# Performance work log

Measured on AMD Instinct MI355X. Metric: run time of the kernel, lower is better.

The kernel has to match this reference:

```python
import jax, jax.numpy as jnp
import numpy as np

N_NODES = 102
EDGES = [[0,6],[0,5],[6,8],[5,7],[0,31],[31,32],[32,33],[28,33],[28,29],[29,30],[30,31],[0,43],[40,41],[41,42],[42,43],[43,44],[44,45],[45,46],[46,47],[47,48],[48,49],[49,50],[50,51],[40,51],[40,52],[46,56],[52,53],[53,54],[54,55],[55,56],[56,57],[57,58],[58,59],[52,59],[0,34],[34,35],[35,36],[36,37],[37,38],[38,39],[34,39],[7,60],[60,61],[61,62],[62,63],[63,64],[60,65],[65,66],[66,67],[67,68],[60,69],[69,70],[70,71],[71,72],[60,73],[73,74],[74,75],[75,76],[60,77],[77,78],[78,79],[79,80],[8,81],[81,82],[82,83],[83,84],[84,85],[81,86],[86,87],[87,88],[88,89],[81,90],[90,91],[91,92],[92,93],[81,94],[94,95],[95,96],[96,97],[81,98],[98,99],[99,100],[100,101]]


def _gcn_norm_adj(edge_index):
    # PyG GCNConv: add self-loops, symmetric normalization.
    # deg computed over target (col) index including self-loops.
    row, col = edge_index[0], edge_index[1]
    deg = jnp.zeros((N_NODES,), jnp.float32).at[col].add(1.0) + 1.0  # +1 for self-loop
    dinv = jnp.where(deg > 0, 1.0 / jnp.sqrt(deg), 0.0)
    norm = dinv[row] * dinv[col]
    # out[col] += norm * x[row]  ->  A[col, row] = norm; self-loops on diagonal.
    A = jnp.zeros((N_NODES, N_NODES), jnp.float32).at[col, row].add(norm)
    A = A + jnp.diag(dinv * dinv)
    return A


def setup_inputs() -> dict:
    key = jax.random.key(0)
    k1, k2, k3, k4, k5 = jax.random.split(key, 5)
    B, n = 32, 256
    hidden, embed = 256, 256
    x = jax.random.normal(k1, (B, n, N_NODES * 2), jnp.float32)
    W_gnn = jax.random.normal(k2, (2, hidden), jnp.float32) * 0.5
    b_gnn = jax.random.normal(k3, (hidden,), jnp.float32) * 0.1
    W_proj = jax.random.normal(k4, (hidden, embed), jnp.float32) * (1.0 / np.sqrt(hidden))
    b_proj = jax.random.normal(k5, (embed,), jnp.float32) * 0.1
    edge_index = jnp.asarray(np.array(EDGES, dtype=np.int32).T)  # [2, 84]
    return {"x": x, "W_gnn": W_gnn, "b_gnn": b_gnn,
            "W_proj": W_proj, "b_proj": b_proj, "edge_index": edge_index}


def reference(x, W_gnn, b_gnn, W_proj, b_proj, edge_index):
    B, n, _ = x.shape
    xf = x.reshape(B, n, N_NODES, 2)                      # [B, n, 102, 2]
    A = _gcn_norm_adj(edge_index)                         # [102, 102]
    xw = jnp.einsum('bnuc,ch->bnuh', xf, W_gnn)           # transform
    h = jnp.einsum('vu,bnuh->bnvh', A, xw) + b_gnn        # propagate + bias
    h = jax.nn.relu(h)
    out = jnp.einsum('bnvh,he->bnve', h, W_proj) + b_proj # [B, n, 102, embed]
    return out
```

## Files before the change

### kernel.cpp

```cpp
#include <hip/hip_runtime.h>

#define N_NODES 102
#define NP 8192
#define RBLOCKS 3264
#define RSTRIDE 128

typedef _Float16 f16x8 __attribute__((ext_vector_type(8)));
typedef _Float16 f16x2 __attribute__((ext_vector_type(2)));
typedef float f32x4 __attribute__((ext_vector_type(4)));

__global__ void build_tables(const int* __restrict__ ei, int ne,
                             int4* __restrict__ gtu, float4* __restrict__ gtw) {
    __shared__ int   deg[N_NODES];
    __shared__ float dinv[N_NODES];
    __shared__ int   cnt[N_NODES];
    __shared__ int   tu[N_NODES][4];
    __shared__ float tw[N_NODES][4];
    int t = threadIdx.x;
    if (t < N_NODES) deg[t] = 1;
    __syncthreads();
    if (t == 0) for (int e = 0; e < ne; ++e) deg[ei[ne + e]] += 1;
    __syncthreads();
    if (t < N_NODES) {
        dinv[t] = 1.0f / sqrtf((float)deg[t]);
        cnt[t] = 1;
        for (int j = 0; j < 4; ++j) { tu[t][j] = 2 * t; tw[t][j] = 0.0f; }
    }
    __syncthreads();
    if (t < N_NODES) tw[t][0] = dinv[t] * dinv[t];
    __syncthreads();
    if (t == 0) {
        for (int e = 0; e < ne; ++e) {
            int r = ei[e], c = ei[ne + e];
            int s = cnt[c] < 4 ? cnt[c] : 3;
            cnt[c] = s + 1;
            tu[c][s] = 2 * r;
            tw[c][s] = dinv[r] * dinv[c];
        }
    }
    __syncthreads();
    if (t < N_NODES) {
        gtu[t] = make_int4(tu[t][0], tu[t][1], tu[t][2], tu[t][3]);
        gtw[t] = make_float4(tw[t][0], tw[t][1], tw[t][2], tw[t][3]);
    }
}

__global__ void prep_w(const float* __restrict__ Wp, _Float16* __restrict__ WpT) {
    int tid = blockIdx.x * 256 + threadIdx.x;
    for (int i = tid; i < 65536; i += 16384) {
        int col = i & 255, k = i >> 8;
        WpT[col * 256 + k] = (_Float16)Wp[i];
    }
}

__global__ __launch_bounds__(256, 2) void gnn_main(
    const float* __restrict__ x,
    const _Float16* __restrict__ WpT,
    const int4*  __restrict__ gtu,
    const float4* __restrict__ gtw,
    const float* __restrict__ Wg,
    const float* __restrict__ bg,
    const float* __restrict__ bp,
    float* __restrict__ out)
{
    __shared__ float xs[4 * 2 * N_NODES];
    __shared__ int4   stu[N_NODES];
    __shared__ float4 stw[N_NODES];
    __shared__ _Float16 W0l[256], W1l[256], bgl[256];
    const int tid = threadIdx.x;
    const int w  = tid >> 6;
    const int l  = tid & 63;
    const int qk = l >> 4;
    const int m  = l & 15;
    const int c0  = blockIdx.y * 64;
    const int rbi = blockIdx.x;

    f16x8 bfragR[8][4];
    #pragma unroll
    for (int t = 0; t < 8; ++t)
        #pragma unroll
        for (int nt = 0; nt < 4; ++nt)
            bfragR[t][nt] = *reinterpret_cast<const f16x8*>(
                &WpT[(c0 + nt * 16 + m) * 256 + qk * 8 + 32 * t]);

    if (tid < N_NODES) { stu[tid] = gtu[tid]; stw[tid] = gtw[tid]; }
    W0l[tid] = (_Float16)Wg[tid];
    W1l[tid] = (_Float16)Wg[256 + tid];
    bgl[tid] = (_Float16)bg[tid];

    float bpf[4];
    #pragma unroll
    for (int nt = 0; nt < 4; ++nt) bpf[nt] = bp[c0 + nt * 16 + m];

    const f16x2 z2 = (f16x2){ (_Float16)0.0f, (_Float16)0.0f };

    #pragma unroll 1
    for (int j = 0; j < 26; ++j) {
        const int rb = rbi + j * RSTRIDE;
        if (rb >= RBLOCKS) break;
        const int rowblk = rb * 256;
        const int pbase  = rowblk / N_NODES;

        __syncthreads();
        #pragma unroll
        for (int pi = 0; pi < 4; ++pi) {
            int p = pbase + pi;
            if (tid < 2 * N_NODES)
                xs[pi * 2 * N_NODES + tid] = (p < NP) ? x[(size_t)p * (2 * N_NODES) + tid] : 0.0f;
        }
        __syncthreads();

        f16x2 y0pk[4], y1pk[4];
        #pragma unroll
        for (int s = 0; s < 4; ++s) {
            int r = rowblk + w * 64 + s * 16 + m;
            int p = r / N_NODES;
            int v = r - p * N_NODES;
            const float* xp = &xs[(p - pbase) * 2 * N_NODES];
            int4  U = stu[v];
            float4 W = stw[v];
            float a0 = W.x * xp[U.x]     + W.y * xp[U.y]
                     + W.z * xp[U.z]     + W.w * xp[U.w];
            float a1 = W.x * xp[U.x + 1] + W.y * xp[U.y + 1]
                     + W.z * xp[U.z + 1] + W.w * xp[U.w + 1];
            _Float16 h0 = (_Float16)a0;
            _Float16 h1 = (_Float16)a1;
            y0pk[s] = (f16x2){ h0, h0 };
            y1pk[s] = (f16x2){ h1, h1 };
        }

        f32x4 acc[4][4];
        #pragma unroll
        for (int s = 0; s < 4; ++s)
            #pragma unroll
            for (int nt = 0; nt < 4; ++nt)
                acc[s][nt] = (f32x4){0.f, 0.f, 0.f, 0.f};

        #pragma unroll
        for (int t = 0; t < 8; ++t) {
            const int kk = qk * 8 + 32 * t;
            union { f16x8 v; f16x2 p[4]; } w0u, w1u, bbu;
            w0u.v = *reinterpret_cast<const f16x8*>(&W0l[kk]);
            w1u.v = *reinterpret_cast<const f16x8*>(&W1l[kk]);
            bbu.v = *reinterpret_cast<const f16x8*>(&bgl[kk]);
            #pragma unroll
            for (int s = 0; s < 4; ++s) {
                union { f16x8 v; f16x2 p[4]; } af;
                #pragma unroll
                for (int j2 = 0; j2 < 4; ++j2) {
                    f16x2 h = w0u.p[j2] * y0pk[s] + w1u.p[j2] * y1pk[s] + bbu.p[j2];
                    af.p[j2] = __builtin_elementwise_max(h, z2);
                }
                #pragma unroll
                for (int nt = 0; nt < 4; ++nt)
                    acc[s][nt] = __builtin_amdgcn_mfma_f32_16x16x32_f16(af.v, bfragR[t][nt], acc[s][nt], 0, 0, 0);
            }
        }

        const long rowbase = (long)rowblk + (long)w * 64;
        #pragma unroll
        for (int s = 0; s < 4; ++s) {
            #pragma unroll
            for (int nt = 0; nt < 4; ++nt) {
                const int e = c0 + nt * 16 + m;
                #pragma unroll
                for (int reg = 0; reg < 4; ++reg) {
                    long r = rowbase + s * 16 + qk * 4 + reg;
                    out[r * 256 + e] = acc[s][nt][reg] + bpf[nt];
                }
            }
        }
    }
}

extern "C" void kernel_launch(void* const* d_in, const int* in_sizes, int n_in,
                              void* d_out, int out_size, void* d_ws, size_t ws_size,
                              hipStream_t stream) {
    const float* x  = (const float*)d_in[0];
    const float* Wg = (const float*)d_in[1];
    const float* bg = (const float*)d_in[2];
    const float* Wp = (const float*)d_in[3];
    const float* bp = (const float*)d_in[4];
    const int* ei   = (const int*)d_in[5];
    float* out = (float*)d_out;

    const int ne = in_sizes[5] / 2;

    int4*     gtu = (int4*)d_ws;
    float4*   gtw = (float4*)((char*)d_ws + 2048);
    _Float16* WpT = (_Float16*)((char*)d_ws + 4096);

    build_tables<<<1, 128, 0, stream>>>(ei, ne, gtu, gtw);
    prep_w<<<64, 256, 0, stream>>>(Wp, WpT);

    gnn_main<<<dim3(RSTRIDE, 4), 256, 0, stream>>>(x, WpT, gtu, gtw, Wg, bg, bp, out);
}
```

Measured before the change: 199.5 us.

## Warp-specialize: dedicate one wavefront to double-buffered x prefetch

Splits the block so three wavefronts do compute and MFMA on 192-row blocks while the fourth wavefront prefetches the next x window into a double-buffered LDS area. The per-iteration pair of syncthreads is replaced by a single barrier, so global loads of x overlap with compute. In exchange, a quarter of the wavefronts no longer do compute, giving fewer MFMA rows per block, and there are more iterations per block (34 instead of up to 26).

Result: slower. 284.9 us (+42.8%).

```diff
diff --git a/kernel.cpp b/kernel.cpp
--- a/kernel.cpp
+++ b/kernel.cpp
@@ -2,8 +2,10 @@
 
 #define N_NODES 102
 #define NP 8192
-#define RBLOCKS 3264
-#define RSTRIDE 128
+#define RB192 4352
+#define GRIDX 128
+#define NITER 34
+#define XWIN 612
 
 typedef _Float16 f16x8 __attribute__((ext_vector_type(8)));
 typedef _Float16 f16x2 __attribute__((ext_vector_type(2)));
@@ -63,7 +65,7 @@
     const float* __restrict__ bp,
     float* __restrict__ out)
 {
-    __shared__ float xs[4 * 2 * N_NODES];
+    __shared__ float xsb[2][XWIN];
     __shared__ int4   stu[N_NODES];
     __shared__ float4 stw[N_NODES];
     __shared__ _Float16 W0l[256], W1l[256], bgl[256];
@@ -74,14 +76,17 @@
     const int m  = l & 15;
     const int c0  = blockIdx.y * 64;
     const int rbi = blockIdx.x;
+    const size_t gmax = (size_t)NP * (2 * N_NODES);
 
     f16x8 bfragR[8][4];
-    #pragma unroll
-    for (int t = 0; t < 8; ++t)
+    if (w < 3) {
         #pragma unroll
-        for (int nt = 0; nt < 4; ++nt)
-            bfragR[t][nt] = *reinterpret_cast<const f16x8*>(
-                &WpT[(c0 + nt * 16 + m) * 256 + qk * 8 + 32 * t]);
+        for (int t = 0; t < 8; ++t)
+            #pragma unroll
+            for (int nt = 0; nt < 4; ++nt)
+                bfragR[t][nt] = *reinterpret_cast<const f16x8*>(
+                    &WpT[(c0 + nt * 16 + m) * 256 + qk * 8 + 32 * t]);
+    }
 
     if (tid < N_NODES) { stu[tid] = gtu[tid]; stw[tid] = gtw[tid]; }
     W0l[tid] = (_Float16)Wg[tid];
@@ -92,84 +97,113 @@
     #pragma unroll
     for (int nt = 0; nt < 4; ++nt) bpf[nt] = bp[c0 + nt * 16 + m];
 
+    if (w == 3) {
+        const int pb0 = (rbi * 192) / N_NODES;
+        const size_t gbase = (size_t)pb0 * (2 * N_NODES);
+        #pragma unroll
+        for (int i = 0; i < 10; ++i) {
+            int idx = l + i * 64;
+            if (idx < XWIN)
+                xsb[0][idx] = (gbase + idx < gmax) ? x[gbase + idx] : 0.0f;
+        }
+    }
+    __syncthreads();
+
     const f16x2 z2 = (f16x2){ (_Float16)0.0f, (_Float16)0.0f };
 
     #pragma unroll 1
-    for (int j = 0; j < 26; ++j) {
-        const int rb = rbi + j * RSTRIDE;
-        if (rb >= RBLOCKS) break;
-        const int rowblk = rb * 256;
-        const int pbase  = rowblk / N_NODES;
-
-        __syncthreads();
-        #pragma unroll
-        for (int pi = 0; pi < 4; ++pi) {
-            int p = pbase + pi;
-            if (tid < 2 * N_NODES)
-                xs[pi * 2 * N_NODES + tid] = (p < NP) ? x[(size_t)p * (2 * N_NODES) + tid] : 0.0f;
+    for (int j = 0; j < NITER; ++j) {
+        const int rb = rbi + j * GRIDX;
+        const int cur = j & 1;
+
+        if (w < 3) {
+            const int rowblk = rb * 192;
+            const int pbase  = rowblk / N_NODES;
+            const float* xsw = xsb[cur];
+
+            f16x2 y0pk[4], y1pk[4];
+            #pragma unroll
+            for (int s = 0; s < 4; ++s) {
+                int r = rowblk + w * 64 + s * 16 + m;
+                int p = r / N_NODES;
+                int v = r - p * N_NODES;
+                const float* xp = &xsw[(p - pbase) * 2 * N_NODES];
+                int4  U = stu[v];
+                float4 W = stw[v];
+                float a0 = W.x * xp[U.x]     + W.y * xp[U.y]
+                         + W.z * xp[U.z]     + W.w * xp[U.w];
+                float a1 = W.x * xp[U.x + 1] + W.y * xp[U.y + 1]
+                         + W.z * xp[U.z + 1] + W.w * xp[U.w + 1];
+                _Float16 h0 = (_Float16)a0;
+                _Float16 h1 = (_Float16)a1;
+                y0pk[s] = (f16x2){ h0, h0 };
+                y1pk[s] = (f16x2){ h1, h1 };
+            }
+
+            f32x4 acc[4][4];
+            #pragma unroll
+            for (int s = 0; s < 4; ++s)
+                #pragma unroll
+                for (int nt = 0; nt < 4; ++nt)
+                    acc[s][nt] = (f32x4){0.f, 0.f, 0.f, 0.f};
+
+            #pragma unroll
+            for (int t = 0; t < 8; ++t) {
+                const int kk = qk * 8 + 32 * t;
+                union { f16x8 v; f16x2 p[4]; } w0u, w1u, bbu;
+                w0u.v = *reinterpret_cast<const f16x8*>(&W0l[kk]);
+                w1u.v = *reinterpret_cast<const f16x8*>(&W1l[kk]);
+                bbu.v = *reinterpret_cast<const f16x8*>(&bgl[kk]);
+                #pragma unroll
+                for (int s = 0; s < 4; ++s) {
+                    union { f16x8 v; f16x2 p[4]; } af;
+                    #pragma unroll
+                    for (int j2 = 0; j2 < 4; ++j2) {
+                        f16x2 h = w0u.p[j2] * y0pk[s] + w1u.p[j2] * y1pk[s] + bbu.p[j2];
+                        af.p[j2] = __builtin_elementwise_max(h, z2);
+                    }
+                    #pragma unroll
+                    for (int nt = 0; nt < 4; ++nt)
+                        acc[s][nt] = __builtin_amdgcn_mfma_f32_16x16x32_f16(af.v, bfragR[t][nt], acc[s][nt], 0, 0, 0);
+                }
+            }
+
+            const long rowbase = (long)rowblk + (long)w * 64;
+            #pragma unroll
+            for (int s = 0; s < 4; ++s) {
+                #pragma unroll
+                for (int nt = 0; nt < 4; ++nt) {
+                    const int e = c0 + nt * 16 + m;
+                    #pragma unroll
+                    for (int reg = 0; reg < 4; ++reg) {
+                        long r = rowbase + s * 16 + qk * 4 + reg;
+                        out[r * 256 + e] = acc[s][nt][reg] + bpf[nt];
+                    }
+                }
+            }
+        } else {
+            if (j + 1 < NITER) {
+                const int rbn = rbi + (j + 1) * GRIDX;
+                const int pbn = (rbn * 192) / N_NODES;
+                const size_t gbase = (size_t)pbn * (2 * N_NODES);
+                float tmp[10];
+                #pragma unroll
+                for (int i = 0; i < 10; ++i) {
+                    int idx = l + i * 64;
+                    tmp[i] = (idx < XWIN && gbase + idx < gmax) ? x[gbase + idx] : 0.0f;
+                }
+                float* dst = xsb[cur ^ 1];
+                #pragma unroll
+                for (int i = 0; i < 10; ++i) {
+                    int idx = l + i * 64;
+                    if (idx < XWIN) dst[idx] = tmp[i];
+                }
+            }
+            asm volatile("s_waitcnt lgkmcnt(0)" ::: "memory");
         }
-        __syncthreads();
-
-        f16x2 y0pk[4], y1pk[4];
-        #pragma unroll
-        for (int s = 0; s < 4; ++s) {
-            int r = rowblk + w * 64 + s * 16 + m;
-            int p = r / N_NODES;
-            int v = r - p * N_NODES;
-            const float* xp = &xs[(p - pbase) * 2 * N_NODES];
-            int4  U = stu[v];
-            float4 W = stw[v];
-            float a0 = W.x * xp[U.x]     + W.y * xp[U.y]
-                     + W.z * xp[U.z]     + W.w * xp[U.w];
-            float a1 = W.x * xp[U.x + 1] + W.y * xp[U.y + 1]
-                     + W.z * xp[U.z + 1] + W.w * xp[U.w + 1];
-            _Float16 h0 = (_Float16)a0;
-            _Float16 h1 = (_Float16)a1;
-            y0pk[s] = (f16x2){ h0, h0 };
-            y1pk[s] = (f16x2){ h1, h1 };
-        }
-
-        f32x4 acc[4][4];
-        #pragma unroll
-        for (int s = 0; s < 4; ++s)
-            #pragma unroll
-            for (int nt = 0; nt < 4; ++nt)
-                acc[s][nt] = (f32x4){0.f, 0.f, 0.f, 0.f};
-
-        #pragma unroll
-        for (int t = 0; t < 8; ++t) {
-            const int kk = qk * 8 + 32 * t;
-            union { f16x8 v; f16x2 p[4]; } w0u, w1u, bbu;
-            w0u.v = *reinterpret_cast<const f16x8*>(&W0l[kk]);
-            w1u.v = *reinterpret_cast<const f16x8*>(&W1l[kk]);
-            bbu.v = *reinterpret_cast<const f16x8*>(&bgl[kk]);
-            #pragma unroll
-            for (int s = 0; s < 4; ++s) {
-                union { f16x8 v; f16x2 p[4]; } af;
-                #pragma unroll
-                for (int j2 = 0; j2 < 4; ++j2) {
-                    f16x2 h = w0u.p[j2] * y0pk[s] + w1u.p[j2] * y1pk[s] + bbu.p[j2];
-                    af.p[j2] = __builtin_elementwise_max(h, z2);
-                }
-                #pragma unroll
-                for (int nt = 0; nt < 4; ++nt)
-                    acc[s][nt] = __builtin_amdgcn_mfma_f32_16x16x32_f16(af.v, bfragR[t][nt], acc[s][nt], 0, 0, 0);
-            }
-        }
-
-        const long rowbase = (long)rowblk + (long)w * 64;
-        #pragma unroll
-        for (int s = 0; s < 4; ++s) {
-            #pragma unroll
-            for (int nt = 0; nt < 4; ++nt) {
-                const int e = c0 + nt * 16 + m;
-                #pragma unroll
-                for (int reg = 0; reg < 4; ++reg) {
-                    long r = rowbase + s * 16 + qk * 4 + reg;
-                    out[r * 256 + e] = acc[s][nt][reg] + bpf[nt];
-                }
-            }
-        }
+
+        __builtin_amdgcn_s_barrier();
+        asm volatile("" ::: "memory");
     }
 }
 
@@ -193,5 +227,5 @@
     build_tables<<<1, 128, 0, stream>>>(ei, ne, gtu, gtw);
     prep_w<<<64, 256, 0, stream>>>(Wp, WpT);
 
-    gnn_main<<<dim3(RSTRIDE, 4), 256, 0, stream>>>(x, WpT, gtu, gtw, Wg, bg, bp, out);
-}
+    gnn_main<<<dim3(GRIDX, 4), 256, 0, stream>>>(x, WpT, gtu, gtw, Wg, bg, bp, out);
+}
```

## Double-buffer x tiles in LDS with async global_load_lds prefetch

Applied to the files above, without the earlier changes.

The per-iteration synchronous x staging, which needed two block barriers, is replaced by a double-buffered LDS tile. Each wave issues a direct global-to-LDS 16-byte load for the next iteration's node features while the current tile is being computed. One barrier per iteration remains, guarded by a permissive vmcnt wait that relies on in-order completion of the previous iteration's outstanding stores. The aim is to hide x load latency, at the cost of doubled LDS for x and a subtle dependence on memory counter ordering.

After: 203.4 us. About the same (+1.9%).

```diff
diff --git a/kernel.cpp b/kernel.cpp
--- a/kernel.cpp
+++ b/kernel.cpp
@@ -8,6 +8,10 @@
 typedef _Float16 f16x8 __attribute__((ext_vector_type(8)));
 typedef _Float16 f16x2 __attribute__((ext_vector_type(2)));
 typedef float f32x4 __attribute__((ext_vector_type(4)));
+
+#define GLOAD_LDS16(src, dst) \
+    __builtin_amdgcn_global_load_lds((const __attribute__((address_space(1))) void*)(src), \
+                                     (__attribute__((address_space(3))) void*)(dst), 16, 0, 0)
 
 __global__ void build_tables(const int* __restrict__ ei, int ne,
                              int4* __restrict__ gtu, float4* __restrict__ gtw) {
@@ -63,7 +67,7 @@
     const float* __restrict__ bp,
     float* __restrict__ out)
 {
-    __shared__ float xs[4 * 2 * N_NODES];
+    __shared__ float xsb[2][4 * 2 * N_NODES];
     __shared__ int4   stu[N_NODES];
     __shared__ float4 stw[N_NODES];
     __shared__ _Float16 W0l[256], W1l[256], bgl[256];
@@ -92,6 +96,14 @@
     #pragma unroll
     for (int nt = 0; nt < 4; ++nt) bpf[nt] = bp[c0 + nt * 16 + m];
 
+    {
+        const int pb0 = (rbi * 256) / N_NODES;
+        if (pb0 + w < NP && l < 51)
+            GLOAD_LDS16(x + (size_t)(pb0 + w) * (2 * N_NODES) + l * 4,
+                        &xsb[0][w * (2 * N_NODES)]);
+    }
+    __syncthreads();
+
     const f16x2 z2 = (f16x2){ (_Float16)0.0f, (_Float16)0.0f };
 
     #pragma unroll 1
@@ -100,23 +112,30 @@
         if (rb >= RBLOCKS) break;
         const int rowblk = rb * 256;
         const int pbase  = rowblk / N_NODES;
-
-        __syncthreads();
-        #pragma unroll
-        for (int pi = 0; pi < 4; ++pi) {
-            int p = pbase + pi;
-            if (tid < 2 * N_NODES)
-                xs[pi * 2 * N_NODES + tid] = (p < NP) ? x[(size_t)p * (2 * N_NODES) + tid] : 0.0f;
-        }
-        __syncthreads();
-
+        const int cur = j & 1;
+
+        asm volatile("s_waitcnt vmcnt(63)" ::: "memory");
+        __builtin_amdgcn_s_barrier();
+        __builtin_amdgcn_sched_barrier(0);
+
+        {
+            const int rbn = rbi + (j + 1) * RSTRIDE;
+            if (rbn < RBLOCKS) {
+                const int pbn = (rbn * 256) / N_NODES;
+                if (pbn + w < NP && l < 51)
+                    GLOAD_LDS16(x + (size_t)(pbn + w) * (2 * N_NODES) + l * 4,
+                                &xsb[cur ^ 1][w * (2 * N_NODES)]);
+            }
+        }
+
+        const float* xsw = xsb[cur];
         f16x2 y0pk[4], y1pk[4];
         #pragma unroll
         for (int s = 0; s < 4; ++s) {
             int r = rowblk + w * 64 + s * 16 + m;
             int p = r / N_NODES;
             int v = r - p * N_NODES;
-            const float* xp = &xs[(p - pbase) * 2 * N_NODES];
+            const float* xp = &xsw[(p - pbase) * 2 * N_NODES];
             int4  U = stu[v];
             float4 W = stw[v];
             float a0 = W.x * xp[U.x]     + W.y * xp[U.y]
```
